# Performance work log

Hardware: AMD Instinct MI355X
Metric: run time of the kernel (lower is better)

Reference implementation:

```python
import jax, jax.numpy as jnp
import numpy as np

B, N, E, D, R, O, L = 256, 128, 2048, 512, 1024, 10, 5


def setup_inputs() -> dict:
    key = jax.random.key(0)
    k0, k1, k2, k3, k4 = jax.random.split(key, 5)
    x = jax.random.normal(k0, (B, N, D), jnp.float32)
    edges = jax.random.randint(k1, (B, 2, E), 0, N)  # per-graph COO (src,dst)
    xav = (6.0 / (D + 1 + R)) ** 0.5  # xavier_uniform for cp-pool W
    W_cp = jax.random.uniform(k2, (L, D + 1, R), jnp.float32, -xav, xav)
    lin_w = jax.random.normal(k3, (L, R, O), jnp.float32) * 0.03
    lin_b = jax.random.normal(k4, (L, O), jnp.float32) * 0.01
    return {"x": x, "edges": edges, "W_cp": W_cp, "lin_w": lin_w, "lin_b": lin_b}


def _cp_pool(h, W):
    # graph_cp_pooling: append ones column, tanh(x @ W), prod over nodes
    ones = jnp.ones(h.shape[:-1] + (1,), h.dtype)
    hn = jnp.concatenate([h, ones], axis=-1)  # [B, N, D+1]
    fea = jnp.tanh(jnp.einsum('bnd,dr->bnr', hn, W))  # [B, N, R]
    return jnp.prod(fea, axis=1)  # [B, R]


def _aggregate(h, src, dst):
    # pooled = (I + A) @ h  with sum neighbor pooling (learn_eps=False)
    gathered = jnp.take_along_axis(h, src[..., None], axis=1)  # [B, E, D]
    b_idx = jnp.arange(h.shape[0])[:, None]  # [B, 1]
    agg = jnp.zeros_like(h).at[b_idx, dst].add(gathered)  # scatter-add to dst
    return h + agg


def reference(x, edges, W_cp, lin_w, lin_b):
    src, dst = edges[:, 0], edges[:, 1]
    h = x
    # layer 0 readout on raw features (dropout is identity in eval mode)
    score = _cp_pool(h, W_cp[0]) @ lin_w[0] + lin_b[0]
    for layer in range(1, L):
        h = _aggregate(h, src, dst)
        score = score + _cp_pool(h, W_cp[layer]) @ lin_w[layer] + lin_b[layer]
    return score  # [B, O]
```

## Files before the change

### kernel.cpp

```cpp
#include <hip/hip_runtime.h>
#include <math.h>

#define B 256
#define N 128
#define E 2048
#define D 512
#define R 1024
#define O 10
#define L 5
#define BK 32

typedef unsigned short u16;
typedef unsigned int u32;
typedef __bf16 bf16x8 __attribute__((ext_vector_type(8)));
typedef u16 u16x8 __attribute__((ext_vector_type(8)));
typedef float floatx4 __attribute__((ext_vector_type(4)));

__device__ inline u16 f2bf(float f) {
    union { float f; u32 u; } v; v.f = f;
    u32 u = v.u;
    return (u16)((u + 0x7fffu + ((u >> 16) & 1u)) >> 16);
}
__device__ inline float bf2f(u16 s) {
    union { u32 u; float f; } v; v.u = ((u32)s) << 16;
    return v.f;
}

__device__ inline float fast_tanh(float x) {
    return 1.0f - 2.0f / (__expf(2.0f * x) + 1.0f);
}

__device__ inline void gload16(const void* g, void* l) {
    __builtin_amdgcn_global_load_lds(
        (const __attribute__((address_space(1))) void*)g,
        (__attribute__((address_space(3))) void*)l, 16, 0, 0);
}

__device__ inline bf16x8 ldsfrag(const u16* p) {
    u16x8 v = *(const u16x8*)p;
    return __builtin_bit_cast(bf16x8, v);
}

__global__ void zero_kernel(float* __restrict__ p, size_t n) {
    size_t i = (size_t)blockIdx.x * blockDim.x + threadIdx.x;
    size_t stride = (size_t)gridDim.x * blockDim.x;
    for (; i < n; i += stride) p[i] = 0.f;
}

__global__ void fill_adj_kernel(const int* __restrict__ edges, float* __restrict__ C) {
    int idx = blockIdx.x * blockDim.x + threadIdx.x;
    if (idx >= B * E) return;
    int b = idx / E;
    int e = idx - b * E;
    int src = edges[b * 2 * E + e];
    int dst = edges[b * 2 * E + E + e];
    atomicAdd(&C[(size_t)b * N * N + (size_t)dst * N + src], 1.0f);
}

__global__ void diag_kernel(float* __restrict__ C) {
    int idx = blockIdx.x * blockDim.x + threadIdx.x;
    if (idx >= B * N) return;
    C[(size_t)(idx >> 7) * N * N + (size_t)(idx & 127) * 129] += 1.0f;
}

__global__ void cbf_kernel(const float4* __restrict__ C4, ushort4* __restrict__ o, size_t n4) {
    size_t i = (size_t)blockIdx.x * blockDim.x + threadIdx.x;
    size_t stride = (size_t)gridDim.x * blockDim.x;
    for (; i < n4; i += stride) {
        float4 v = C4[i];
        ushort4 r;
        r.x = f2bf(v.x); r.y = f2bf(v.y); r.z = f2bf(v.z); r.w = f2bf(v.w);
        o[i] = r;
    }
}

__global__ void split_kernel(const float4* __restrict__ x4,
                             uint2* __restrict__ hi4, uint2* __restrict__ lo4, size_t n4) {
    size_t i = (size_t)blockIdx.x * blockDim.x + threadIdx.x;
    size_t stride = (size_t)gridDim.x * blockDim.x;
    for (; i < n4; i += stride) {
        float4 v = x4[i];
        u16 h0 = f2bf(v.x), h1 = f2bf(v.y), h2 = f2bf(v.z), h3 = f2bf(v.w);
        uint2 hp; hp.x = (u32)h0 | ((u32)h1 << 16); hp.y = (u32)h2 | ((u32)h3 << 16);
        hi4[i] = hp;
        u16 l0 = f2bf(v.x - bf2f(h0)), l1 = f2bf(v.y - bf2f(h1));
        u16 l2 = f2bf(v.z - bf2f(h2)), l3 = f2bf(v.w - bf2f(h3));
        uint2 lp; lp.x = (u32)l0 | ((u32)l1 << 16); lp.y = (u32)l2 | ((u32)l3 << 16);
        lo4[i] = lp;
    }
}

__global__ __launch_bounds__(256)
void wt_split_kernel(const float* __restrict__ W_cp,
                     u16* __restrict__ Wt_hi, u16* __restrict__ Wt_lo) {
    __shared__ float t[64][65];
    const int l = blockIdx.z, k0 = blockIdx.y * 64, r0 = blockIdx.x * 64;
    const float* Wl = W_cp + (size_t)l * 513 * 1024;
    const int tx = threadIdx.x & 63, ty = threadIdx.x >> 6;
#pragma unroll
    for (int p = 0; p < 16; ++p) {
        int k = ty + p * 4;
        t[k][tx] = Wl[(size_t)(k0 + k) * 1024 + r0 + tx];
    }
    __syncthreads();
    u16* oh = Wt_hi + ((size_t)l * 1024 + r0) * 512 + k0;
    u16* ol = Wt_lo + ((size_t)l * 1024 + r0) * 512 + k0;
#pragma unroll
    for (int p = 0; p < 16; ++p) {
        int r = ty + p * 4;
        float v = t[tx][r];
        u16 hv = f2bf(v);
        oh[(size_t)r * 512 + tx] = hv;
        ol[(size_t)r * 512 + tx] = f2bf(v - bf2f(hv));
    }
}

__global__ __launch_bounds__(512, 2)
void cp_pool_mfma_kernel(const u16* __restrict__ h_hi, const u16* __restrict__ h_lo,
                         const u16* __restrict__ Wt_hi, const u16* __restrict__ Wt_lo,
                         const float* __restrict__ Wbias,
                         float* __restrict__ prod_out)
{
    __shared__ u16 SS[4][256 * BK];

    const int flat = blockIdx.x;
    const int xcd  = flat & 7;
    const int idx  = flat >> 3;
    const int bp   = xcd * 16 + (idx >> 2);
    const int r0   = (idx & 3) * 256;

    const int tid  = threadIdx.x;
    const int w    = tid >> 6;
    const int lane = tid & 63;
    const int rb   = w & 3;
    const int cb   = w >> 2;

    floatx4 acc[4][8];
#pragma unroll
    for (int i = 0; i < 4; ++i)
#pragma unroll
        for (int j = 0; j < 8; ++j)
#pragma unroll
            for (int k = 0; k < 4; ++k) acc[i][j][k] = 0.f;

    const int lrow = lane >> 2;
    const int g8   = (((lane & 3) ^ ((lane >> 3) & 3)) * 8);
    const u16* gA_h = h_hi  + ((size_t)bp * 256 + w * 32 + lrow) * 512 + g8;
    const u16* gA_l = h_lo  + ((size_t)bp * 256 + w * 32 + lrow) * 512 + g8;
    const u16* gB_h = Wt_hi + ((size_t)(r0 + w * 32 + lrow)) * 512 + g8;
    const u16* gB_l = Wt_lo + ((size_t)(r0 + w * 32 + lrow)) * 512 + g8;
    const int ldst = w * 1024 + lane * 8;

    const int am = rb * 64 + (lane & 15);
    const int bn = cb * 128 + (lane & 15);
    const int ko = (((lane >> 4) ^ ((lane >> 1) & 3)) * 8);

#define DMASTEP(ks)                                                            \
    {                                                                          \
        const size_t go = (size_t)(ks) * BK;                                   \
        gload16(gA_h + go, &SS[0][ldst]);                                      \
        gload16(gA_h + go + 16 * 512, &SS[0][ldst + 512]);                     \
        gload16(gA_l + go, &SS[1][ldst]);                                      \
        gload16(gA_l + go + 16 * 512, &SS[1][ldst + 512]);                     \
        gload16(gB_h + go, &SS[2][ldst]);                                      \
        gload16(gB_h + go + 16 * 512, &SS[2][ldst + 512]);                     \
        gload16(gB_l + go, &SS[3][ldst]);                                      \
        gload16(gB_l + go + 16 * 512, &SS[3][ldst + 512]);                     \
    }

    DMASTEP(0)

    for (int ks = 0; ks < 16; ++ks) {
        __syncthreads();

        bf16x8 ah[4], al[4], bh[8], bl[8];
#pragma unroll
        for (int t = 0; t < 4; ++t) {
            ah[t] = ldsfrag(&SS[0][(am + t * 16) * BK + ko]);
            al[t] = ldsfrag(&SS[1][(am + t * 16) * BK + ko]);
        }
#pragma unroll
        for (int t = 0; t < 8; ++t) {
            bh[t] = ldsfrag(&SS[2][(bn + t * 16) * BK + ko]);
            bl[t] = ldsfrag(&SS[3][(bn + t * 16) * BK + ko]);
        }
        __syncthreads();

        if (ks < 15) DMASTEP(ks + 1)

#pragma unroll
        for (int i = 0; i < 4; ++i)
#pragma unroll
            for (int j = 0; j < 8; ++j) {
                acc[i][j] = __builtin_amdgcn_mfma_f32_16x16x32_bf16(al[i], bh[j], acc[i][j], 0, 0, 0);
                acc[i][j] = __builtin_amdgcn_mfma_f32_16x16x32_bf16(ah[i], bl[j], acc[i][j], 0, 0, 0);
                acc[i][j] = __builtin_amdgcn_mfma_f32_16x16x32_bf16(ah[i], bh[j], acc[i][j], 0, 0, 0);
            }
    }
#undef DMASTEP

    float* red = (float*)&SS[0][0];
    const int quad = lane >> 4;
    const int c16  = lane & 15;
#pragma unroll
    for (int tj = 0; tj < 8; ++tj) {
        const int c = cb * 128 + tj * 16 + c16;
        const float bias = Wbias[r0 + c];
        float p = 1.f;
#pragma unroll
        for (int ti = 0; ti < 4; ++ti)
#pragma unroll
            for (int ri = 0; ri < 4; ++ri)
                p *= fast_tanh(acc[ti][tj][ri] + bias);
        p *= __shfl_xor(p, 16, 64);
        p *= __shfl_xor(p, 32, 64);
        if (quad == 0) red[rb * 256 + c] = p;
    }
    __syncthreads();
    {
        const int t    = tid & 255;
        const int half = tid >> 8;
        const int b    = bp * 2 + half;
        const float v  = red[(half * 2) * 256 + t] * red[(half * 2 + 1) * 256 + t];
        prod_out[(size_t)b * R + r0 + t] = v;
    }
}

__global__ __launch_bounds__(256)
void aggregate_mfma_kernel(const u16* __restrict__ hi_in, const u16* __restrict__ lo_in,
                           const u16* __restrict__ Cbf,
                           u16* __restrict__ hi_out, u16* __restrict__ lo_out)
{
    __shared__ u16 Cs[128 * 32];
    __shared__ u16 Bs_hi[128 * 40];
    __shared__ u16 Bs_lo[128 * 40];

    const int flat = blockIdx.x;
    const int rest = flat >> 3;
    const int b    = (flat & 7) * 32 + (rest >> 2);
    const int d0   = (rest & 3) * 128;

    const int tid  = threadIdx.x;
    const int w    = tid >> 6;
    const int lane = tid & 63;
    const int rb   = w & 1;
    const int cb   = w >> 1;

    floatx4 acc[4][4];
#pragma unroll
    for (int i = 0; i < 4; ++i)
#pragma unroll
        for (int j = 0; j < 4; ++j)
#pragma unroll
            for (int k = 0; k < 4; ++k) acc[i][j][k] = 0.f;

    const int kswz = (((lane & 3) ^ ((lane >> 3) & 3)) * 8);
    const u16* gC = Cbf + ((size_t)b * 128 + (w * 32 + (lane >> 2))) * 128 + kswz;

    const int ssi = tid >> 3;
    const int dg  = (tid & 7) * 16;
    const u16* gBh = hi_in + ((size_t)b * 128 + ssi) * 512 + d0 + dg;
    const u16* gBl = lo_in + ((size_t)b * 128 + ssi) * 512 + d0 + dg;

    const int am  = rb * 64 + (lane & 15);
    const int ko  = (((lane >> 4) ^ ((lane >> 1) & 3)) * 8);
    const int bko = (lane >> 4) * 8;

    for (int s0 = 0; s0 < 128; s0 += 32) {
#pragma unroll
        for (int it = 0; it < 2; ++it)
            gload16(gC + s0 + (size_t)it * 16 * 128, Cs + (w * 2 + it) * 512);

        {
            const u16* ph = gBh + (size_t)s0 * 512;
            const u16* pl = gBl + (size_t)s0 * 512;
            uint4 a0 = *(const uint4*)ph;
            uint4 a1 = *(const uint4*)(ph + 8);
            uint4 b0 = *(const uint4*)pl;
            uint4 b1 = *(const uint4*)(pl + 8);
            const u16* av0 = (const u16*)&a0; const u16* av1 = (const u16*)&a1;
            const u16* bv0 = (const u16*)&b0; const u16* bv1 = (const u16*)&b1;
#pragma unroll
            for (int i = 0; i < 8; ++i) {
                Bs_hi[(dg + i) * 40 + ssi]     = av0[i];
                Bs_hi[(dg + 8 + i) * 40 + ssi] = av1[i];
                Bs_lo[(dg + i) * 40 + ssi]     = bv0[i];
                Bs_lo[(dg + 8 + i) * 40 + ssi] = bv1[i];
            }
        }
        __syncthreads();

        bf16x8 af[4], bhf[4], blf[4];
#pragma unroll
        for (int t = 0; t < 4; ++t) {
            af[t]  = ldsfrag(&Cs[(am + t * 16) * 32 + ko]);
            const int d = cb * 64 + t * 16 + (lane & 15);
            bhf[t] = ldsfrag(&Bs_hi[d * 40 + bko]);
            blf[t] = ldsfrag(&Bs_lo[d * 40 + bko]);
        }
#pragma unroll
        for (int i = 0; i < 4; ++i)
#pragma unroll
            for (int j = 0; j < 4; ++j) {
                acc[i][j] = __builtin_amdgcn_mfma_f32_16x16x32_bf16(af[i], bhf[j], acc[i][j], 0, 0, 0);
                acc[i][j] = __builtin_amdgcn_mfma_f32_16x16x32_bf16(af[i], blf[j], acc[i][j], 0, 0, 0);
            }
        __syncthreads();
    }

    const int quad = lane >> 4;
    const int c16  = lane & 15;
#pragma unroll
    for (int i = 0; i < 4; ++i)
#pragma unroll
        for (int j = 0; j < 4; ++j) {
            const int d = d0 + cb * 64 + j * 16 + c16;
#pragma unroll
            for (int ri = 0; ri < 4; ++ri) {
                const int n = rb * 64 + i * 16 + quad * 4 + ri;
                size_t o = ((size_t)b * 128 + n) * 512 + d;
                float v = acc[i][j][ri];
                u16 hv = f2bf(v);
                hi_out[o] = hv;
                lo_out[o] = f2bf(v - bf2f(hv));
            }
        }
}

__global__ __launch_bounds__(256)
void score_kernel(const float* __restrict__ prod,
                  const float* __restrict__ lin_w,
                  const float* __restrict__ lin_b,
                  float* __restrict__ out)
{
    const int b   = blockIdx.x;
    const int tid = threadIdx.x;

    float acc[O];
#pragma unroll
    for (int o = 0; o < O; ++o) acc[o] = 0.f;

    for (int l = 0; l < L; ++l) {
        const float* pl = prod + ((size_t)l * B + b) * R;
        const float* wl = lin_w + (size_t)l * R * O;
        for (int r = tid; r < R; r += 256) {
            const float p = pl[r];
#pragma unroll
            for (int o = 0; o < O; ++o)
                acc[o] = fmaf(p, wl[r * O + o], acc[o]);
        }
    }

    __shared__ float sb[256];
    for (int o = 0; o < O; ++o) {
        sb[tid] = acc[o];
        __syncthreads();
        for (int off = 128; off > 0; off >>= 1) {
            if (tid < off) sb[tid] += sb[tid + off];
            __syncthreads();
        }
        if (tid == 0) {
            float bias = 0.f;
            for (int l = 0; l < L; ++l) bias += lin_b[l * O + o];
            out[b * O + o] = sb[0] + bias;
        }
        __syncthreads();
    }
}

extern "C" void kernel_launch(void* const* d_in, const int* in_sizes, int n_in,
                              void* d_out, int out_size, void* d_ws, size_t ws_size,
                              hipStream_t stream) {
    const float* x     = (const float*)d_in[0];
    const int*   edges = (const int*)d_in[1];
    const float* W_cp  = (const float*)d_in[2];
    const float* lin_w = (const float*)d_in[3];
    const float* lin_b = (const float*)d_in[4];
    float*       out   = (float*)d_out;

    char* ws = (char*)d_ws;
    const size_t C_BYTES   = (size_t)B * N * N * 4;
    const size_t CBF_BYTES = (size_t)B * N * N * 2;
    const size_t HH_BYTES  = (size_t)B * N * D * 2;
    const size_t WT_BYTES  = (size_t)L * 1024 * 512 * 2;

    float* C     = (float*)ws;                    ws += C_BYTES;
    u16*   Cbf   = (u16*)ws;                      ws += CBF_BYTES;
    u16*   hiA   = (u16*)ws;                      ws += HH_BYTES;
    u16*   loA   = (u16*)ws;                      ws += HH_BYTES;
    u16*   hiB   = (u16*)ws;                      ws += HH_BYTES;
    u16*   loB   = (u16*)ws;                      ws += HH_BYTES;
    u16*   Wt_hi = (u16*)ws;                      ws += WT_BYTES;
    u16*   Wt_lo = (u16*)ws;                      ws += WT_BYTES;
    float* prod  = (float*)ws;

    zero_kernel<<<1024, 256, 0, stream>>>(C, (size_t)B * N * N);
    fill_adj_kernel<<<(B * E + 255) / 256, 256, 0, stream>>>(edges, C);
    diag_kernel<<<(B * N + 255) / 256, 256, 0, stream>>>(C);
    cbf_kernel<<<1024, 256, 0, stream>>>((const float4*)C, (ushort4*)Cbf,
                                         (size_t)B * N * N / 4);
    wt_split_kernel<<<dim3(16, 8, L), 256, 0, stream>>>(W_cp, Wt_hi, Wt_lo);
    split_kernel<<<2048, 256, 0, stream>>>((const float4*)x, (uint2*)hiA, (uint2*)loA,
                                           (size_t)B * N * D / 4);

    cp_pool_mfma_kernel<<<512, 512, 0, stream>>>(
        hiA, loA, Wt_hi, Wt_lo, W_cp + (size_t)512 * 1024, prod);

    const u16* phi = hiA; const u16* plo = loA;
    u16* bhi[2] = {hiB, hiA};
    u16* blo[2] = {loB, loA};
    for (int l = 1; l < L; ++l) {
        u16* nhi = bhi[(l - 1) & 1];
        u16* nlo = blo[(l - 1) & 1];
        aggregate_mfma_kernel<<<1024, 256, 0, stream>>>(phi, plo, Cbf, nhi, nlo);
        cp_pool_mfma_kernel<<<512, 512, 0, stream>>>(
            nhi, nlo,
            Wt_hi + (size_t)l * 1024 * 512, Wt_lo + (size_t)l * 1024 * 512,
            W_cp + ((size_t)l * 513 + 512) * 1024,
            prod + (size_t)l * B * R);
        phi = nhi; plo = nlo;
    }

    score_kernel<<<B, 256, 0, stream>>>(prod, lin_w, lin_b, out);
}
```

Before: 748.1 us.

## Double-buffer LDS tiles in cp_pool MFMA kernel to overlap loads with compute

Moves the cp_pool kernel's shared-memory staging into a two-stage ping-pong buffer in dynamic LDS of 128 KB per block. The next K-slice is fetched while the current one is read into registers and fed to MFMA, which removes one barrier per iteration. The cost is doubled LDS use: the kernel still declares launch_bounds(512,2), but 128 KB per block likely allows only one block per CU. That may reduce occupancy and latency hiding.

```diff
diff --git a/kernel.cpp b/kernel.cpp
--- a/kernel.cpp
+++ b/kernel.cpp
@@ -121,7 +121,7 @@
                          const float* __restrict__ Wbias,
                          float* __restrict__ prod_out)
 {
-    __shared__ u16 SS[4][256 * BK];
+    extern __shared__ u16 SS[];
 
     const int flat = blockIdx.x;
     const int xcd  = flat & 7;
@@ -155,38 +155,40 @@
     const int bn = cb * 128 + (lane & 15);
     const int ko = (((lane >> 4) ^ ((lane >> 1) & 3)) * 8);
 
-#define DMASTEP(ks)                                                            \
+#define DMASTEP(ks, bufofs)                                                    \
     {                                                                          \
         const size_t go = (size_t)(ks) * BK;                                   \
-        gload16(gA_h + go, &SS[0][ldst]);                                      \
-        gload16(gA_h + go + 16 * 512, &SS[0][ldst + 512]);                     \
-        gload16(gA_l + go, &SS[1][ldst]);                                      \
-        gload16(gA_l + go + 16 * 512, &SS[1][ldst + 512]);                     \
-        gload16(gB_h + go, &SS[2][ldst]);                                      \
-        gload16(gB_h + go + 16 * 512, &SS[2][ldst + 512]);                     \
-        gload16(gB_l + go, &SS[3][ldst]);                                      \
-        gload16(gB_l + go + 16 * 512, &SS[3][ldst + 512]);                     \
-    }
-
-    DMASTEP(0)
-
+        gload16(gA_h + go,            &SS[(bufofs) + 0 * 8192 + ldst]);        \
+        gload16(gA_h + go + 16 * 512, &SS[(bufofs) + 0 * 8192 + ldst + 512]);  \
+        gload16(gA_l + go,            &SS[(bufofs) + 1 * 8192 + ldst]);        \
+        gload16(gA_l + go + 16 * 512, &SS[(bufofs) + 1 * 8192 + ldst + 512]);  \
+        gload16(gB_h + go,            &SS[(bufofs) + 2 * 8192 + ldst]);        \
+        gload16(gB_h + go + 16 * 512, &SS[(bufofs) + 2 * 8192 + ldst + 512]);  \
+        gload16(gB_l + go,            &SS[(bufofs) + 3 * 8192 + ldst]);        \
+        gload16(gB_l + go + 16 * 512, &SS[(bufofs) + 3 * 8192 + ldst + 512]);  \
+    }
+
+    DMASTEP(0, 0)
+
+#pragma unroll
     for (int ks = 0; ks < 16; ++ks) {
+        const int po = (ks & 1) * 32768;
         __syncthreads();
 
+        if (ks < 15) DMASTEP(ks + 1, 32768 - po)
+
+        const u16* S0 = &SS[po];
         bf16x8 ah[4], al[4], bh[8], bl[8];
 #pragma unroll
         for (int t = 0; t < 4; ++t) {
-            ah[t] = ldsfrag(&SS[0][(am + t * 16) * BK + ko]);
-            al[t] = ldsfrag(&SS[1][(am + t * 16) * BK + ko]);
+            ah[t] = ldsfrag(&S0[0 * 8192 + (am + t * 16) * BK + ko]);
+            al[t] = ldsfrag(&S0[1 * 8192 + (am + t * 16) * BK + ko]);
         }
 #pragma unroll
         for (int t = 0; t < 8; ++t) {
-            bh[t] = ldsfrag(&SS[2][(bn + t * 16) * BK + ko]);
-            bl[t] = ldsfrag(&SS[3][(bn + t * 16) * BK + ko]);
-        }
-        __syncthreads();
-
-        if (ks < 15) DMASTEP(ks + 1)
+            bh[t] = ldsfrag(&S0[2 * 8192 + (bn + t * 16) * BK + ko]);
+            bl[t] = ldsfrag(&S0[3 * 8192 + (bn + t * 16) * BK + ko]);
+        }
 
 #pragma unroll
         for (int i = 0; i < 4; ++i)
@@ -199,7 +201,7 @@
     }
 #undef DMASTEP
 
-    float* red = (float*)&SS[0][0];
+    float* red = (float*)&SS[0];
     const int quad = lane >> 4;
     const int c16  = lane & 15;
 #pragma unroll
@@ -394,6 +396,9 @@
     u16*   Wt_lo = (u16*)ws;                      ws += WT_BYTES;
     float* prod  = (float*)ws;
 
+    (void)hipFuncSetAttribute((const void*)cp_pool_mfma_kernel,
+                              hipFuncAttributeMaxDynamicSharedMemorySize, 131072);
+
     zero_kernel<<<1024, 256, 0, stream>>>(C, (size_t)B * N * N);
     fill_adj_kernel<<<(B * E + 255) / 256, 256, 0, stream>>>(edges, C);
     diag_kernel<<<(B * N + 255) / 256, 256, 0, stream>>>(C);
@@ -403,7 +408,7 @@
     split_kernel<<<2048, 256, 0, stream>>>((const float4*)x, (uint2*)hiA, (uint2*)loA,
                                            (size_t)B * N * D / 4);
 
-    cp_pool_mfma_kernel<<<512, 512, 0, stream>>>(
+    cp_pool_mfma_kernel<<<512, 512, 131072, stream>>>(
         hiA, loA, Wt_hi, Wt_lo, W_cp + (size_t)512 * 1024, prod);
 
     const u16* phi = hiA; const u16* plo = loA;
@@ -413,7 +418,7 @@
         u16* nhi = bhi[(l - 1) & 1];
         u16* nlo = blo[(l - 1) & 1];
         aggregate_mfma_kernel<<<1024, 256, 0, stream>>>(phi, plo, Cbf, nhi, nlo);
-        cp_pool_mfma_kernel<<<512, 512, 0, stream>>>(
+        cp_pool_mfma_kernel<<<512, 512, 131072, stream>>>(
             nhi, nlo,
             Wt_hi + (size_t)l * 1024 * 512, Wt_lo + (size_t)l * 1024 * 512,
             W_cp + ((size_t)l * 513 + 512) * 1024,
```

Measured after the change: 739.3 us. About the same (-1.2%).
